# Kernel tuning notes

Hardware: AMD Instinct MI355X
Metric: run time of the kernel (lower is better)

Reference implementation:

```python
import jax, jax.numpy as jnp
import numpy as np

KH = KW = 3
STRIDE = 1
PAD = 1
DIL = 1


def setup_inputs() -> dict:
    key = jax.random.key(0)
    k1, k2, k3 = jax.random.split(key, 3)
    x = jax.random.normal(k1, (4, 256, 80, 80), dtype=jnp.float32)
    offset = jax.random.normal(k2, (4, 18, 80, 80), dtype=jnp.float32)
    weight = jax.random.normal(k3, (256, 256, 3, 3), dtype=jnp.float32) * 0.05
    return {"x": x, "offset": offset, "weight": weight}


def _deform_conv(x, offset, weight):
    # Naive deformable conv: bilinear-sample each of the kh*kw kernel taps at
    # (regular grid location + learned offset), then a dense GEMM with weight.
    # Sampling uses grid_sample semantics with align_corners=True (the torch
    # code normalizes by (L-1)/2) and zeros padding -> pure pixel coordinates.
    N, C, H, W = x.shape
    oh, ow = offset.shape[2], offset.shape[3]
    kk = KH * KW
    # offset layout: (N, dg=1, kh, kw, 2, oh, ow); channel 0 = y, 1 = x
    off = offset.reshape(N, KH, KW, 2, oh, ow)
    off_y = off[:, :, :, 0].reshape(N, kk, oh, ow)
    off_x = off[:, :, :, 1].reshape(N, kk, oh, ow)

    ky, kx = jnp.meshgrid(jnp.arange(KH), jnp.arange(KW), indexing='ij')
    ky = (ky.reshape(kk) * DIL).astype(x.dtype)
    kx = (kx.reshape(kk) * DIL).astype(x.dtype)
    base_y = jnp.arange(oh, dtype=x.dtype) * STRIDE - PAD  # [oh]
    base_x = jnp.arange(ow, dtype=x.dtype) * STRIDE - PAD  # [ow]

    # absolute sampling coords, [N, kk, oh, ow]
    py = off_y + ky[None, :, None, None] + base_y[None, None, :, None]
    px = off_x + kx[None, :, None, None] + base_x[None, None, None, :]

    x0 = jnp.floor(px)
    y0 = jnp.floor(py)
    x1 = x0 + 1.0
    y1 = y0 + 1.0
    wx1 = px - x0
    wx0 = 1.0 - wx1
    wy1 = py - y0
    wy0 = 1.0 - wy1

    x_flat = x.reshape(N, C, H * W)

    def corner(xc, yc, w):
        # zeros padding: out-of-bounds corners contribute 0
        m = ((xc >= 0) & (xc <= W - 1) & (yc >= 0) & (yc <= H - 1)).astype(x.dtype)
        xi = jnp.clip(xc, 0, W - 1).astype(jnp.int32)
        yi = jnp.clip(yc, 0, H - 1).astype(jnp.int32)
        idx = yi * W + xi  # [N, kk, oh, ow]
        g = jax.vmap(lambda f, i: f[:, i])(x_flat, idx)  # [N, C, kk, oh, ow]
        return g * (w * m)[:, None]

    sampled = (corner(x0, y0, wx0 * wy0) + corner(x1, y0, wx1 * wy0)
               + corner(x0, y1, wx0 * wy1) + corner(x1, y1, wx1 * wy1))

    OC = weight.shape[0]
    # weight flattens as (oc, c, kh, kw) -> (oc, c*kk); sampled matches (c, kk)
    out = jnp.einsum('of,nfp->nop', weight.reshape(OC, C * kk),
                     sampled.reshape(N, C * kk, oh * ow))
    return out.reshape(N, OC, oh, ow)


def reference(x, offset, weight):
    return _deform_conv(x, offset, weight)
```

## Files before the change

### kernel.cpp

```cpp
#include <hip/hip_runtime.h>


typedef short short8 __attribute__((ext_vector_type(8)));
typedef float floatx4 __attribute__((ext_vector_type(4)));
typedef unsigned int uint4v __attribute__((ext_vector_type(4)));

#define Cc    256
#define OCc   256
#define Hh    80
#define Ww    80
#define HW    6400
#define KK    9
#define Ktot  2304
#define PT    64
#define KC    64
#define NCHUNK (Ktot / KC)
#define NKB   (Ktot / 32)
#define WP_ELEMS (Ktot * OCc)
#define XT_OFF   ((size_t)WP_ELEMS)

#define BARRIER_LDS()                                      \
  do {                                                     \
    asm volatile("s_waitcnt lgkmcnt(0)" ::: "memory");     \
    __builtin_amdgcn_s_barrier();                          \
  } while (0)

__device__ __forceinline__ unsigned short f2bf(float f) {
  unsigned u = __float_as_uint(f);
  u += 0x7FFF + ((u >> 16) & 1);
  return (unsigned short)(u >> 16);
}
__device__ __forceinline__ float bf2f(unsigned short u) {
  return __uint_as_float((unsigned)u << 16);
}
__device__ __forceinline__ unsigned int cvtpk(float lo, float hi) {
  unsigned int r;
  asm("v_cvt_pk_bf16_f32 %0, %1, %2" : "=v"(r) : "v"(lo), "v"(hi));
  return r;
}

__global__ void pack_weight(const float* __restrict__ w,
                            unsigned short* __restrict__ wp) {
  const int t = blockIdx.x * 256 + threadIdx.x;
  const int lane = t & 63;
  const int ocf  = (t >> 6) & 15;
  const int kb   = t >> 10;
  const int oc   = ocf * 16 + (lane & 15);
  const int k0   = kb * 32 + (lane >> 4) * 8;
  const int tap  = k0 >> 8;
  const int c0   = k0 & 255;
  const float* src = w + (size_t)oc * Ktot + (size_t)c0 * KK + tap;
  short8 pk;
  #pragma unroll
  for (int e = 0; e < 8; ++e) pk[e] = (short)f2bf(src[e * KK]);
  *(short8*)(wp + (size_t)t * 8) = pk;
}

__global__ void nhwc_pack(const float* __restrict__ x,
                          unsigned short* __restrict__ xt) {
  __shared__ float tile[64][65];
  const int tid = threadIdx.x;
  const int hw0 = blockIdx.x * 64;
  const int c0  = blockIdx.y * 64;
  const int n   = blockIdx.z;
  #pragma unroll
  for (int i = 0; i < 16; ++i) {
    const int idx = i * 256 + tid;
    const int cl = idx >> 6, hl = idx & 63;
    tile[cl][hl] = x[((size_t)(n * Cc + c0 + cl)) * HW + hw0 + hl];
  }
  __syncthreads();
  #pragma unroll
  for (int i = 0; i < 16; ++i) {
    const int idx = i * 256 + tid;
    const int hl = idx >> 6, cl = idx & 63;
    xt[((size_t)(n * HW + hw0 + hl)) * Cc + c0 + cl] = f2bf(tile[cl][hl]);
  }
}

__global__ __launch_bounds__(512, 4) void dcn_mfma(
    const float* __restrict__ x, const float* __restrict__ offset,
    const unsigned short* __restrict__ wp,
    const unsigned short* __restrict__ xt, float* __restrict__ out) {
  __shared__ unsigned short s_col[3][PT * KC];
  __shared__ float4 s_w[KK * PT];
  __shared__ int4   s_i[KK * PT];

  const int tid  = threadIdx.x;
  const int lane = tid & 63;
  const int wv   = tid >> 6;

  const int bid  = blockIdx.x;
  const int logical = (bid & 7) * 50 + (bid >> 3);
  const int nn   = logical / 100;
  const int tile = logical - nn * 100;
  const int p0   = tile * PT;
  const char* xn = (const char*)(xt + (size_t)nn * HW * Cc);

  for (int s = tid; s < KK * PT; s += 512) {
    const int k = s / PT, p = s % PT;
    const int pp = p0 + p;
    const int oy = pp / Ww, ox = pp % Ww;
    const int ky = k / 3, kx = k % 3;
    const float offy = offset[(size_t)(nn * 18 + 2 * k    ) * HW + pp];
    const float offx = offset[(size_t)(nn * 18 + 2 * k + 1) * HW + pp];
    const float py = offy + (float)(ky + oy - 1);
    const float px = offx + (float)(kx + ox - 1);
    const float fy0 = floorf(py), fx0 = floorf(px);
    const int iy0 = (int)fy0, ix0 = (int)fx0;
    const float wy1 = py - fy0, wx1 = px - fx0;
    const float wy0 = 1.f - wy1, wx0 = 1.f - wx1;
    const bool my0 = (iy0     >= 0) & (iy0     < Hh);
    const bool my1 = (iy0 + 1 >= 0) & (iy0 + 1 < Hh);
    const bool mx0 = (ix0     >= 0) & (ix0     < Ww);
    const bool mx1 = (ix0 + 1 >= 0) & (ix0 + 1 < Ww);
    const int cy0 = min(max(iy0,     0), Hh - 1);
    const int cy1 = min(max(iy0 + 1, 0), Hh - 1);
    const int cx0 = min(max(ix0,     0), Ww - 1);
    const int cx1 = min(max(ix0 + 1, 0), Ww - 1);
    float4 w4;
    w4.x = wx0 * wy0 * ((my0 && mx0) ? 1.f : 0.f);
    w4.y = wx1 * wy0 * ((my0 && mx1) ? 1.f : 0.f);
    w4.z = wx0 * wy1 * ((my1 && mx0) ? 1.f : 0.f);
    w4.w = wx1 * wy1 * ((my1 && mx1) ? 1.f : 0.f);
    int4 i4;
    i4.x = (cy0 * Ww + cx0) * 512;  i4.y = (cy0 * Ww + cx1) * 512;
    i4.z = (cy1 * Ww + cx0) * 512;  i4.w = (cy1 * Ww + cx1) * 512;
    s_w[s] = w4;
    s_i[s] = i4;
  }

  floatx4 acc[2][4] = {};
  const int lm = lane & 15, lg = lane >> 4;
  const int spx = tid >> 3;
  const int cg  = tid & 7;
  const int wbyte = spx * 128 + ((cg * 16) ^ ((spx & 7) << 4));
  __syncthreads();

  short8 raA, rbA, rcA, rdA, raB, rbB, rcB, rdB;
  short8 fA00, fA01, fA10, fA11, fB00, fB01, fB10, fB11;

  #define ISSUE(ch, S)                                                  \
    { const int tap_ = (ch) >> 2;                                       \
      const int coff_ = (((ch) & 3) * KC + cg * 8) * 2;                 \
      const int4 i4_ = s_i[tap_ * PT + spx];                            \
      ra##S = *(const short8*)(xn + i4_.x + coff_);                     \
      rb##S = *(const short8*)(xn + i4_.y + coff_);                     \
      rc##S = *(const short8*)(xn + i4_.z + coff_);                     \
      rd##S = *(const short8*)(xn + i4_.w + coff_); }

  #define PREFA(ch, S)                                                  \
    { const unsigned short* w0_ = wp + (size_t)((ch) * 2) * (16 * 64 * 8) \
                                     + (size_t)((wv * 2) * 64 + lane) * 8; \
      f##S##00 = *(const short8*)(w0_);                                 \
      f##S##01 = *(const short8*)(w0_ + 64 * 8);                        \
      f##S##10 = *(const short8*)(w0_ + 16 * 64 * 8);                   \
      f##S##11 = *(const short8*)(w0_ + 16 * 64 * 8 + 64 * 8); }

  #define FINISH(ch, S)                                                 \
    { const int tap_ = (ch) >> 2;                                       \
      const float4 w4_ = s_w[tap_ * PT + spx];                          \
      float v_[8];                                                      \
      _Pragma("unroll")                                                 \
      for (int e = 0; e < 8; ++e) {                                     \
        v_[e] = w4_.x * bf2f((unsigned short)ra##S[e])                  \
              + w4_.y * bf2f((unsigned short)rb##S[e])                  \
              + w4_.z * bf2f((unsigned short)rc##S[e])                  \
              + w4_.w * bf2f((unsigned short)rd##S[e]);                 \
      }                                                                 \
      uint4v pk_;                                                       \
      _Pragma("unroll")                                                 \
      for (int r = 0; r < 4; ++r) pk_[r] = cvtpk(v_[2 * r], v_[2 * r + 1]); \
      *(uint4v*)((char*)s_col[(ch) % 3] + wbyte) = pk_; }

  #define MFMA_STEP(ch, S)                                              \
    { const char* base_ = (const char*)s_col[(ch) % 3];                 \
      __builtin_amdgcn_s_setprio(1);                                    \
      _Pragma("unroll")                                                 \
      for (int ks = 0; ks < 2; ++ks) {                                  \
        short8 b_[4];                                                   \
        _Pragma("unroll")                                               \
        for (int j = 0; j < 4; ++j) {                                   \
          const int px_ = j * 16 + lm;                                  \
          const int byte_ = px_ * 128 + (((ks * 64) + lg * 16) ^ ((px_ & 7) << 4)); \
          b_[j] = *(const short8*)(base_ + byte_);                      \
        }                                                               \
        const short8 a0_ = ks ? f##S##10 : f##S##00;                    \
        const short8 a1_ = ks ? f##S##11 : f##S##01;                    \
        _Pragma("unroll")                                               \
        for (int j = 0; j < 4; ++j)                                     \
          acc[0][j] = __builtin_amdgcn_mfma_f32_16x16x32_bf16(a0_, b_[j], acc[0][j], 0, 0, 0); \
        _Pragma("unroll")                                               \
        for (int j = 0; j < 4; ++j)                                     \
          acc[1][j] = __builtin_amdgcn_mfma_f32_16x16x32_bf16(a1_, b_[j], acc[1][j], 0, 0, 0); \
      }                                                                 \
      __builtin_amdgcn_s_setprio(0); }

  PREFA(0, A);
  ISSUE(0, A);
  FINISH(0, A);
  ISSUE(1, A);
  BARRIER_LDS();

  for (int it = 0; it < NCHUNK / 2; ++it) {
    const int ch = it * 2;
    MFMA_STEP(ch, A);
    PREFA(ch + 1, B);
    if (ch + 2 < NCHUNK) ISSUE(ch + 2, B);
    FINISH(ch + 1, A);
    BARRIER_LDS();
    MFMA_STEP(ch + 1, B);
    if (ch + 2 < NCHUNK) PREFA(ch + 2, A);
    if (ch + 3 < NCHUNK) ISSUE(ch + 3, A);
    if (ch + 2 < NCHUNK) FINISH(ch + 2, B);
    BARRIER_LDS();
  }

  #pragma unroll
  for (int f = 0; f < 2; ++f) {
    const int oc = (wv * 2 + f) * 16 + lg * 4;
    #pragma unroll
    for (int j = 0; j < 4; ++j) {
      const int px = p0 + j * 16 + lm;
      #pragma unroll
      for (int r = 0; r < 4; ++r) {
        out[(size_t)(nn * OCc + oc + r) * HW + px] = acc[f][j][r];
      }
    }
  }
}

extern "C" void kernel_launch(void* const* d_in, const int* in_sizes, int n_in,
                              void* d_out, int out_size, void* d_ws, size_t ws_size,
                              hipStream_t stream) {
  const float* x      = (const float*)d_in[0];
  const float* offset = (const float*)d_in[1];
  const float* weight = (const float*)d_in[2];
  float* out = (float*)d_out;
  unsigned short* wp = (unsigned short*)d_ws;
  unsigned short* xt = (unsigned short*)d_ws + XT_OFF;

  pack_weight<<<dim3(NKB * 16 * 64 / 256), dim3(256), 0, stream>>>(weight, wp);
  nhwc_pack<<<dim3(HW / 64, Cc / 64, 4), dim3(256), 0, stream>>>(x, xt);
  dcn_mfma<<<dim3(400), dim3(512), 0, stream>>>(x, offset, wp, xt, out);
}
```

Measured before the change: 72.08 us.

## Halve pixel tile to 32 with 256-thread blocks and 4 OC fragments per wave

Reduces the pixel tile per block from 64 to 32 and the block size from 512 to 256 threads, which doubles the grid to 800 blocks. Each wave now covers 64 output channels (4 fragments) by 32 pixels instead of 32 by 64, so per-wave weight fragment loads double while sampled-column LDS reads halve. The bilinear blend also changes to unpack bf16 pairs with shift and mask and use float2 vector math. More blocks improve CU balance and occupancy, but the packed weights are re-read from global memory more often in total.

```diff
diff --git a/kernel.cpp b/kernel.cpp
--- a/kernel.cpp
+++ b/kernel.cpp
@@ -3,6 +3,7 @@
 
 typedef short short8 __attribute__((ext_vector_type(8)));
 typedef float floatx4 __attribute__((ext_vector_type(4)));
+typedef float floatx2 __attribute__((ext_vector_type(2)));
 typedef unsigned int uint4v __attribute__((ext_vector_type(4)));
 
 #define Cc    256
@@ -12,7 +13,7 @@
 #define HW    6400
 #define KK    9
 #define Ktot  2304
-#define PT    64
+#define PT    32
 #define KC    64
 #define NCHUNK (Ktot / KC)
 #define NKB   (Ktot / 32)
@@ -29,9 +30,6 @@
   unsigned u = __float_as_uint(f);
   u += 0x7FFF + ((u >> 16) & 1);
   return (unsigned short)(u >> 16);
-}
-__device__ __forceinline__ float bf2f(unsigned short u) {
-  return __uint_as_float((unsigned)u << 16);
 }
 __device__ __forceinline__ unsigned int cvtpk(float lo, float hi) {
   unsigned int r;
@@ -78,7 +76,7 @@
   }
 }
 
-__global__ __launch_bounds__(512, 4) void dcn_mfma(
+__global__ __launch_bounds__(256, 4) void dcn_mfma(
     const float* __restrict__ x, const float* __restrict__ offset,
     const unsigned short* __restrict__ wp,
     const unsigned short* __restrict__ xt, float* __restrict__ out) {
@@ -91,13 +89,13 @@
   const int wv   = tid >> 6;
 
   const int bid  = blockIdx.x;
-  const int logical = (bid & 7) * 50 + (bid >> 3);
-  const int nn   = logical / 100;
-  const int tile = logical - nn * 100;
+  const int logical = (bid & 7) * 100 + (bid >> 3);
+  const int nn   = logical / 200;
+  const int tile = logical - nn * 200;
   const int p0   = tile * PT;
   const char* xn = (const char*)(xt + (size_t)nn * HW * Cc);
 
-  for (int s = tid; s < KK * PT; s += 512) {
+  for (int s = tid; s < KK * PT; s += 256) {
     const int k = s / PT, p = s % PT;
     const int pp = p0 + p;
     const int oy = pp / Ww, ox = pp % Ww;
@@ -130,7 +128,7 @@
     s_i[s] = i4;
   }
 
-  floatx4 acc[2][4] = {};
+  floatx4 acc[4][2] = {};
   const int lm = lane & 15, lg = lane >> 4;
   const int spx = tid >> 3;
   const int cg  = tid & 7;
@@ -138,7 +136,7 @@
   __syncthreads();
 
   short8 raA, rbA, rcA, rdA, raB, rbB, rcB, rdB;
-  short8 fA00, fA01, fA10, fA11, fB00, fB01, fB10, fB11;
+  short8 fA[2][4], fB[2][4];
 
   #define ISSUE(ch, S)                                                  \
     { const int tap_ = (ch) >> 2;                                       \
@@ -150,49 +148,60 @@
       rd##S = *(const short8*)(xn + i4_.w + coff_); }
 
   #define PREFA(ch, S)                                                  \
-    { const unsigned short* w0_ = wp + (size_t)((ch) * 2) * (16 * 64 * 8) \
-                                     + (size_t)((wv * 2) * 64 + lane) * 8; \
-      f##S##00 = *(const short8*)(w0_);                                 \
-      f##S##01 = *(const short8*)(w0_ + 64 * 8);                        \
-      f##S##10 = *(const short8*)(w0_ + 16 * 64 * 8);                   \
-      f##S##11 = *(const short8*)(w0_ + 16 * 64 * 8 + 64 * 8); }
+    { _Pragma("unroll")                                                 \
+      for (int ks_ = 0; ks_ < 2; ++ks_) {                               \
+        const unsigned short* w0_ = wp                                  \
+            + (size_t)((ch) * 2 + ks_) * (16 * 64 * 8)                  \
+            + (size_t)((wv * 4) * 64 + lane) * 8;                       \
+        _Pragma("unroll")                                               \
+        for (int f_ = 0; f_ < 4; ++f_)                                  \
+          f##S[ks_][f_] = *(const short8*)(w0_ + (size_t)f_ * 64 * 8);  \
+      } }
 
   #define FINISH(ch, S)                                                 \
     { const int tap_ = (ch) >> 2;                                       \
       const float4 w4_ = s_w[tap_ * PT + spx];                          \
-      float v_[8];                                                      \
-      _Pragma("unroll")                                                 \
-      for (int e = 0; e < 8; ++e) {                                     \
-        v_[e] = w4_.x * bf2f((unsigned short)ra##S[e])                  \
-              + w4_.y * bf2f((unsigned short)rb##S[e])                  \
-              + w4_.z * bf2f((unsigned short)rc##S[e])                  \
-              + w4_.w * bf2f((unsigned short)rd##S[e]);                 \
-      }                                                                 \
+      const uint4v ua_ = __builtin_bit_cast(uint4v, ra##S);             \
+      const uint4v ub_ = __builtin_bit_cast(uint4v, rb##S);             \
+      const uint4v uc_ = __builtin_bit_cast(uint4v, rc##S);             \
+      const uint4v ud_ = __builtin_bit_cast(uint4v, rd##S);             \
       uint4v pk_;                                                       \
       _Pragma("unroll")                                                 \
-      for (int r = 0; r < 4; ++r) pk_[r] = cvtpk(v_[2 * r], v_[2 * r + 1]); \
+      for (int r_ = 0; r_ < 4; ++r_) {                                  \
+        floatx2 va_, vb_, vc_, vd_;                                     \
+        va_[0] = __uint_as_float(ua_[r_] << 16);                        \
+        va_[1] = __uint_as_float(ua_[r_] & 0xFFFF0000u);                \
+        vb_[0] = __uint_as_float(ub_[r_] << 16);                        \
+        vb_[1] = __uint_as_float(ub_[r_] & 0xFFFF0000u);                \
+        vc_[0] = __uint_as_float(uc_[r_] << 16);                        \
+        vc_[1] = __uint_as_float(uc_[r_] & 0xFFFF0000u);                \
+        vd_[0] = __uint_as_float(ud_[r_] << 16);                        \
+        vd_[1] = __uint_as_float(ud_[r_] & 0xFFFF0000u);                \
+        const floatx2 v_ = w4_.x * va_ + w4_.y * vb_                    \
+                         + w4_.z * vc_ + w4_.w * vd_;                   \
+        pk_[r_] = cvtpk(v_[0], v_[1]);                                  \
+      }                                                                 \
       *(uint4v*)((char*)s_col[(ch) % 3] + wbyte) = pk_; }
 
   #define MFMA_STEP(ch, S)                                              \
     { const char* base_ = (const char*)s_col[(ch) % 3];                 \
       __builtin_amdgcn_s_setprio(1);                                    \
       _Pragma("unroll")                                                 \
-      for (int ks = 0; ks < 2; ++ks) {                                  \
-        short8 b_[4];                                                   \
+      for (int ks_ = 0; ks_ < 2; ++ks_) {                               \
+        short8 b_[2];                                                   \
         _Pragma("unroll")                                               \
-        for (int j = 0; j < 4; ++j) {                                   \
-          const int px_ = j * 16 + lm;                                  \
-          const int byte_ = px_ * 128 + (((ks * 64) + lg * 16) ^ ((px_ & 7) << 4)); \
-          b_[j] = *(const short8*)(base_ + byte_);                      \
+        for (int j_ = 0; j_ < 2; ++j_) {                                \
+          const int px_ = j_ * 16 + lm;                                 \
+          const int byte_ = px_ * 128 + (((ks_ * 64) + lg * 16) ^ ((px_ & 7) << 4)); \
+          b_[j_] = *(const short8*)(base_ + byte_);                     \
         }                                                               \
-        const short8 a0_ = ks ? f##S##10 : f##S##00;                    \
-        const short8 a1_ = ks ? f##S##11 : f##S##01;                    \
         _Pragma("unroll")                                               \
-        for (int j = 0; j < 4; ++j)                                     \
-          acc[0][j] = __builtin_amdgcn_mfma_f32_16x16x32_bf16(a0_, b_[j], acc[0][j], 0, 0, 0); \
-        _Pragma("unroll")                                               \
-        for (int j = 0; j < 4; ++j)                                     \
-          acc[1][j] = __builtin_amdgcn_mfma_f32_16x16x32_bf16(a1_, b_[j], acc[1][j], 0, 0, 0); \
+        for (int f_ = 0; f_ < 4; ++f_) {                                \
+          _Pragma("unroll")                                             \
+          for (int j_ = 0; j_ < 2; ++j_)                                \
+            acc[f_][j_] = __builtin_amdgcn_mfma_f32_16x16x32_bf16(      \
+                f##S[ks_][f_], b_[j_], acc[f_][j_], 0, 0, 0);           \
+        }                                                               \
       }                                                                 \
       __builtin_amdgcn_s_setprio(0); }
 
@@ -217,10 +226,10 @@
   }
 
   #pragma unroll
-  for (int f = 0; f < 2; ++f) {
-    const int oc = (wv * 2 + f) * 16 + lg * 4;
+  for (int f = 0; f < 4; ++f) {
+    const int oc = (wv * 4 + f) * 16 + lg * 4;
     #pragma unroll
-    for (int j = 0; j < 4; ++j) {
+    for (int j = 0; j < 2; ++j) {
       const int px = p0 + j * 16 + lm;
       #pragma unroll
       for (int r = 0; r < 4; ++r) {
@@ -242,5 +251,5 @@
 
   pack_weight<<<dim3(NKB * 16 * 64 / 256), dim3(256), 0, stream>>>(weight, wp);
   nhwc_pack<<<dim3(HW / 64, Cc / 64, 4), dim3(256), 0, stream>>>(x, xt);
-  dcn_mfma<<<dim3(400), dim3(512), 0, stream>>>(x, offset, wp, xt, out);
-}
+  dcn_mfma<<<dim3(800), dim3(256), 0, stream>>>(x, offset, wp, xt, out);
+}
```

New measurement: 85.54 us. 18.7% more time.
